# Kernel optimization log

Measured on AMD Instinct MI355X. Metric: run time of the kernel, lower is better.

Reference implementation:

```python
import jax, jax.numpy as jnp
import numpy as np

DIM = 768
HEADS = 12
HEAD_DIM = DIM // HEADS
SCALE = HEAD_DIM ** -0.5


def setup_inputs() -> dict:
    key = jax.random.key(0)
    ks = jax.random.split(key, 6)
    B, N, M, C = 4, 2048, 1024, DIM
    x = jax.random.normal(ks[0], (B, N, C), dtype=jnp.float32)
    r = jax.random.normal(ks[1], (B, M, C), dtype=jnp.float32)
    s = 1.0 / np.sqrt(C)
    W_q = jax.random.normal(ks[2], (C, C), dtype=jnp.float32) * s
    W_kv = jax.random.normal(ks[3], (C, 2 * C), dtype=jnp.float32) * s
    W_proj = jax.random.normal(ks[4], (C, C), dtype=jnp.float32) * s
    b_proj = jax.random.normal(ks[5], (C,), dtype=jnp.float32) * 0.02
    return {"x": x, "r": r, "W_q": W_q, "W_kv": W_kv, "W_proj": W_proj, "b_proj": b_proj}


def reference(x, r, W_q, W_kv, W_proj, b_proj):
    B, N, C = x.shape
    _, M, _ = r.shape
    H, D = HEADS, C // HEADS
    # projections (no bias on q/kv per qkv_bias=False)
    q = (x @ W_q).reshape(B, N, H, D)            # bnhd
    kv = (r @ W_kv).reshape(B, M, 2, H, D)
    k = kv[:, :, 0]                               # bmhd
    v = kv[:, :, 1]                               # bmhd
    attn = jnp.einsum('bnhd,bmhd->bhnm', q, k) * SCALE
    attn = jax.nn.softmax(attn, axis=-1)
    out = jnp.einsum('bhnm,bmhd->bnhd', attn, v).reshape(B, N, C)
    return out @ W_proj + b_proj
```

## Files before the change

### kernel.cpp

```cpp
#include <hip/hip_runtime.h>
#include <hip/hip_bf16.h>
#include <cstdint>

#define HEADS 12

typedef __attribute__((ext_vector_type(8))) __bf16 bf16x8;
typedef __attribute__((ext_vector_type(4))) __bf16 bf16x4;
typedef __attribute__((ext_vector_type(4))) float f32x4;
typedef __attribute__((ext_vector_type(16))) float f32x16;

#define AS1 __attribute__((address_space(1)))
#define AS3 __attribute__((address_space(3)))

__device__ __forceinline__ void gload16(const void* src, void* lds) {
  __builtin_amdgcn_global_load_lds((AS1 void*)src, (AS3 void*)lds, 16, 0, 0);
}

__device__ __forceinline__ uint32_t cvtpk(float lo, float hi) {
  uint32_t r;
  asm("v_cvt_pk_bf16_f32 %0, %1, %2" : "=v"(r) : "v"(lo), "v"(hi));
  return r;
}

__device__ __forceinline__ float exp2_fast(float x) {
  float r;
  asm("v_exp_f32 %0, %1" : "=v"(r) : "v"(x));
  return r;
}

__global__ void k_cast2(const float* __restrict__ x, const float* __restrict__ r,
                        __bf16* __restrict__ xb, __bf16* __restrict__ rb) {
  int i = (blockIdx.x * 256 + threadIdx.x) * 4;
  const float* src;
  __bf16* dst;
  int off;
  if (i < 6291456) { src = x; dst = xb; off = i; }
  else             { src = r; dst = rb; off = i - 6291456; }
  float4 v = *(const float4*)(src + off);
  bf16x4 o;
  o[0] = (__bf16)v.x; o[1] = (__bf16)v.y; o[2] = (__bf16)v.z; o[3] = (__bf16)v.w;
  *(bf16x4*)(dst + off) = o;
}

__global__ void k_twc3(const float* __restrict__ Wq, const float* __restrict__ Wkv,
                       const float* __restrict__ Wp, __bf16* __restrict__ wqt,
                       __bf16* __restrict__ wkvt, __bf16* __restrict__ wpt) {
  __shared__ float tile[32][33];
  const float* W; __bf16* Wt; int N; float scale;
  if (blockIdx.z == 0)      { W = Wq;  Wt = wqt;  N = 768;  scale = 0.18033688011112042f; }
  else if (blockIdx.z == 1) { W = Wkv; Wt = wkvt; N = 1536; scale = 1.0f; }
  else                      { W = Wp;  Wt = wpt;  N = 768;  scale = 1.0f; }
  int nt = blockIdx.x, kt = blockIdx.y;
  if (nt * 32 >= N) return;
  int c = threadIdx.x & 31, r0 = threadIdx.x >> 5;
#pragma unroll
  for (int i = 0; i < 4; ++i) {
    int r = r0 + i * 8;
    tile[r][c] = W[(size_t)(kt * 32 + r) * N + nt * 32 + c];
  }
  __syncthreads();
#pragma unroll
  for (int i = 0; i < 4; ++i) {
    int r = r0 + i * 8;
    Wt[(size_t)(nt * 32 + r) * 768 + kt * 32 + c] = (__bf16)(tile[c][r] * scale);
  }
}

__global__ __launch_bounds__(256, 2) void k_gemm12(
    const __bf16* __restrict__ xb, const __bf16* __restrict__ rb,
    const __bf16* __restrict__ wqt, const __bf16* __restrict__ wkvt,
    __bf16* __restrict__ qb, __bf16* __restrict__ kbp, __bf16* __restrict__ vbp) {
  __shared__ __align__(16) char ldsA[2][16384];
  __shared__ __align__(16) char ldsB[2][16384];
  const int tid = threadIdx.x;
  const int ln = tid & 63;
  const int w = tid >> 6;
  int id = blockIdx.x;
  id = (id & 7) * 96 + (id >> 3);
  const __bf16* A; const __bf16* Bt; int bm0, bn0; bool qpart;
  if (id < 384) { A = xb; Bt = wqt;  bm0 = (id / 6) * 128;  bn0 = (id % 6) * 128;  qpart = true; }
  else { int i2 = id - 384; A = rb; Bt = wkvt; bm0 = (i2 / 12) * 128; bn0 = (i2 % 12) * 128; qpart = false; }
  const int wm0 = (w >> 1) * 64, wn0 = (w & 1) * 64;

  auto stage = [&](char* lds, const __bf16* G, int row0, int k0) {
    const char* gb = (const char*)(G + (size_t)row0 * 768 + k0);
#pragma unroll
    for (int c = 0; c < 4; ++c) {
      int off = c * 4096 + tid * 16;
      int row = off >> 7;
      int s = ((off >> 4) & 7) ^ (row & 7);
      gload16(gb + (size_t)row * 1536 + (s << 4), lds + c * 4096 + (w << 10));
    }
  };

  f32x4 acc[4][4] = {};
  stage(ldsA[0], A, bm0, 0);
  stage(ldsB[0], Bt, bn0, 0);
  __syncthreads();
  for (int kt = 0; kt < 12; ++kt) {
    const char* bufA = ldsA[kt & 1];
    const char* bufB = ldsB[kt & 1];
    if (kt + 1 < 12) {
      stage(ldsA[(kt + 1) & 1], A, bm0, (kt + 1) << 6);
      stage(ldsB[(kt + 1) & 1], Bt, bn0, (kt + 1) << 6);
    }
    bf16x8 af[2][4], bf[2][4];
#pragma unroll
    for (int kk = 0; kk < 2; ++kk)
#pragma unroll
      for (int mt = 0; mt < 4; ++mt) {
        int row = wm0 + mt * 16 + (ln & 15);
        af[kk][mt] = *(const bf16x8*)(bufA + row * 128 + (((kk * 4 + (ln >> 4)) ^ (row & 7)) << 4));
      }
#pragma unroll
    for (int kk = 0; kk < 2; ++kk)
#pragma unroll
      for (int nt = 0; nt < 4; ++nt) {
        int row = wn0 + nt * 16 + (ln & 15);
        bf[kk][nt] = *(const bf16x8*)(bufB + row * 128 + (((kk * 4 + (ln >> 4)) ^ (row & 7)) << 4));
      }
    __builtin_amdgcn_s_setprio(1);
#pragma unroll
    for (int kk = 0; kk < 2; ++kk)
#pragma unroll
      for (int mt = 0; mt < 4; ++mt)
#pragma unroll
        for (int nt = 0; nt < 4; ++nt)
          acc[mt][nt] = __builtin_amdgcn_mfma_f32_16x16x32_bf16(af[kk][mt], bf[kk][nt], acc[mt][nt], 0, 0, 0);
    __builtin_amdgcn_s_setprio(0);
    __syncthreads();
  }

  char* ldsT = &ldsA[0][0];
  const bool vpart = (!qpart) && (bn0 >= 768);
  if (!vpart) {
#pragma unroll
    for (int mt = 0; mt < 4; ++mt)
#pragma unroll
      for (int nt = 0; nt < 4; ++nt)
#pragma unroll
        for (int jj = 0; jj < 4; ++jj) {
          int rowl = wm0 + mt * 16 + ((ln >> 4) << 2) + jj;
          int colb = (wn0 + nt * 16 + (ln & 15)) * 2;
          *(__bf16*)(ldsT + rowl * 256 + (colb ^ ((rowl & 7) << 4))) = (__bf16)acc[mt][nt][jj];
        }
  } else {
#pragma unroll
    for (int mt = 0; mt < 4; ++mt)
#pragma unroll
      for (int nt = 0; nt < 4; ++nt)
#pragma unroll
        for (int jj = 0; jj < 4; ++jj) {
          int dloc = wn0 + nt * 16 + (ln & 15);
          int kvb = (wm0 + mt * 16 + ((ln >> 4) << 2) + jj) * 2;
          *(__bf16*)(ldsT + dloc * 256 + (kvb ^ ((dloc & 7) << 4))) = (__bf16)acc[mt][nt][jj];
        }
  }
  __syncthreads();

  if (qpart) {
#pragma unroll
    for (int it = 0; it < 8; ++it) {
      int rowl = it * 16 + (tid >> 4);
      int colb = (tid & 15) * 16;
      bf16x8 v = *(const bf16x8*)(ldsT + rowl * 256 + (colb ^ ((rowl & 7) << 4)));
      *(bf16x8*)(qb + (size_t)(bm0 + rowl) * 768 + bn0 + (tid & 15) * 8) = v;
    }
  } else if (!vpart) {
    const int bb = bm0 >> 10, kvb0 = (bm0 & 1023) >> 5, hh0 = bn0 >> 6;
#pragma unroll
    for (int it = 0; it < 8; ++it) {
      int hh = it >> 2, t32 = it & 3;
      int dc = tid >> 5, kvl = tid & 31;
      int rowl = t32 * 32 + kvl;
      int colb = hh * 128 + (dc >> 1) * 32 + (dc & 1) * 16;
      bf16x8 v = *(const bf16x8*)(ldsT + rowl * 256 + (colb ^ ((rowl & 7) << 4)));
      *(bf16x8*)(kbp + ((size_t)(bb * 12 + hh0 + hh) * 32 + kvb0 + t32) * 2048 + tid * 8) = v;
    }
  } else {
    const int bb = bm0 >> 10, kvb0 = (bm0 & 1023) >> 5, hh0 = (bn0 - 768) >> 6;
#pragma unroll
    for (int it = 0; it < 8; ++it) {
      int hh = it >> 2, t32 = it & 3;
      int d = ((tid >> 7) << 5) + (tid & 31);
      int kvl8 = (((tid >> 6) & 1) << 4) + (((tid >> 5) & 1) << 3);
      int dloc = hh * 64 + d;
      int kvb = (t32 * 32 + kvl8) * 2;
      bf16x8 v = *(const bf16x8*)(ldsT + dloc * 256 + (kvb ^ ((dloc & 7) << 4)));
      *(bf16x8*)(vbp + ((size_t)(bb * 12 + hh0 + hh) * 32 + kvb0 + t32) * 2048 + tid * 8) = v;
    }
  }
}

__global__ __launch_bounds__(256, 2) void k_gemmP(
    const __bf16* __restrict__ A, const __bf16* __restrict__ Bt,
    float* __restrict__ C, const float* __restrict__ bias) {
  __shared__ __align__(16) char ldsA[2][16384];
  __shared__ __align__(16) char ldsB[2][16384];
  const int tid = threadIdx.x;
  const int ln = tid & 63;
  const int w = tid >> 6;
  int bid = blockIdx.y * 6 + blockIdx.x;
  bid = (bid & 7) * 48 + (bid >> 3);
  const int bm0 = (bid / 6) * 128, bn0 = (bid % 6) * 128;
  const int wm0 = (w >> 1) * 64, wn0 = (w & 1) * 64;

  auto stage = [&](char* lds, const __bf16* G, int row0, int k0) {
    const char* gb = (const char*)(G + (size_t)row0 * 768 + k0);
#pragma unroll
    for (int c = 0; c < 4; ++c) {
      int off = c * 4096 + tid * 16;
      int row = off >> 7;
      int s = ((off >> 4) & 7) ^ (row & 7);
      gload16(gb + (size_t)row * 1536 + (s << 4), lds + c * 4096 + (w << 10));
    }
  };

  f32x4 acc[4][4] = {};
  stage(ldsA[0], A, bm0, 0);
  stage(ldsB[0], Bt, bn0, 0);
  __syncthreads();
  for (int kt = 0; kt < 12; ++kt) {
    const char* bufA = ldsA[kt & 1];
    const char* bufB = ldsB[kt & 1];
    if (kt + 1 < 12) {
      stage(ldsA[(kt + 1) & 1], A, bm0, (kt + 1) << 6);
      stage(ldsB[(kt + 1) & 1], Bt, bn0, (kt + 1) << 6);
    }
    bf16x8 af[2][4], bf[2][4];
#pragma unroll
    for (int kk = 0; kk < 2; ++kk)
#pragma unroll
      for (int mt = 0; mt < 4; ++mt) {
        int row = wm0 + mt * 16 + (ln & 15);
        af[kk][mt] = *(const bf16x8*)(bufA + row * 128 + (((kk * 4 + (ln >> 4)) ^ (row & 7)) << 4));
      }
#pragma unroll
    for (int kk = 0; kk < 2; ++kk)
#pragma unroll
      for (int nt = 0; nt < 4; ++nt) {
        int row = wn0 + nt * 16 + (ln & 15);
        bf[kk][nt] = *(const bf16x8*)(bufB + row * 128 + (((kk * 4 + (ln >> 4)) ^ (row & 7)) << 4));
      }
    __builtin_amdgcn_s_setprio(1);
#pragma unroll
    for (int kk = 0; kk < 2; ++kk)
#pragma unroll
      for (int mt = 0; mt < 4; ++mt)
#pragma unroll
        for (int nt = 0; nt < 4; ++nt)
          acc[mt][nt] = __builtin_amdgcn_mfma_f32_16x16x32_bf16(af[kk][mt], bf[kk][nt], acc[mt][nt], 0, 0, 0);
    __builtin_amdgcn_s_setprio(0);
    __syncthreads();
  }
#pragma unroll
  for (int mt = 0; mt < 4; ++mt) {
    int row = bm0 + wm0 + mt * 16 + ((ln >> 4) << 2);
#pragma unroll
    for (int nt = 0; nt < 4; ++nt) {
      int col = bn0 + wn0 + nt * 16 + (ln & 15);
      float bv = bias[col];
#pragma unroll
      for (int jj = 0; jj < 4; ++jj)
        C[(size_t)(row + jj) * 768 + col] = acc[mt][nt][jj] + bv;
    }
  }
}

__global__ __launch_bounds__(128, 3) void k_attn(
    const __bf16* __restrict__ q, const __bf16* __restrict__ kb,
    const __bf16* __restrict__ vb, __bf16* __restrict__ ao) {
  __shared__ __align__(16) char ldsK[3][8192];
  const int tid = threadIdx.x, ln = tid & 63;
  const int l5 = ln >> 5, l32 = ln & 31, w = tid >> 6;
  int id = blockIdx.x;
  id = (id & 7) * 192 + (id >> 3);
  const int qt = id & 31, bh = id >> 5;
  const int b = bh / HEADS, h = bh % HEADS;
  const int qrow = b * 2048 + qt * 64 + w * 32 + l32;

  const char* kbase = (const char*)kb + (size_t)bh * 131072;
  const __bf16* vbase = vb + (size_t)bh * 65536;
  const int vchunk = l5 * 256 + l32 * 8;

  auto stageK = [&](int t, int buf) {
#pragma unroll
    for (int c = 0; c < 4; ++c)
      gload16(kbase + (size_t)t * 8192 + c * 2048 + tid * 16, ldsK[buf] + c * 2048 + tid * 16);
  };

  bf16x8 qf[4];
#pragma unroll
  for (int s = 0; s < 4; ++s)
    qf[s] = *(const bf16x8*)(q + (size_t)qrow * 768 + h * 64 + 16 * s + 8 * l5);

  stageK(0, 0);
  stageK(1, 1);

  f32x16 accO[2] = {};
  float mrow = -1e30f, lrow = 0.f;

  asm volatile("s_waitcnt vmcnt(0)" ::: "memory");
  __builtin_amdgcn_s_barrier();

  for (int t = 0; t < 16; ++t) {
    const char* bufK = ldsK[t % 3];

    bf16x8 vf[2][2][2];
    {
      const __bf16* vt = vbase + (size_t)(2 * t) * 2048 + vchunk;
#pragma unroll
      for (int nt = 0; nt < 2; ++nt)
#pragma unroll
        for (int dt = 0; dt < 2; ++dt)
#pragma unroll
          for (int ks = 0; ks < 2; ++ks)
            vf[nt][dt][ks] = *(const bf16x8*)(vt + nt * 2048 + (dt * 2 + ks) * 512);
    }
    if (t < 14) stageK(t + 2, (t + 2) % 3);

    f32x16 s16[2] = {};
    __builtin_amdgcn_s_setprio(1);
#pragma unroll
    for (int s = 0; s < 4; ++s) {
      bf16x8 kf0 = *(const bf16x8*)(bufK + (s * 2 + l5) * 512 + l32 * 16);
      s16[0] = __builtin_amdgcn_mfma_f32_32x32x16_bf16(kf0, qf[s], s16[0], 0, 0, 0);
      bf16x8 kf1 = *(const bf16x8*)(bufK + 4096 + (s * 2 + l5) * 512 + l32 * 16);
      s16[1] = __builtin_amdgcn_mfma_f32_32x32x16_bf16(kf1, qf[s], s16[1], 0, 0, 0);
    }
    __builtin_amdgcn_s_setprio(0);

    float lm = s16[0][0];
#pragma unroll
    for (int nt = 0; nt < 2; ++nt)
#pragma unroll
      for (int i = 0; i < 16; ++i) lm = fmaxf(lm, s16[nt][i]);
    if (!__all(lm <= mrow + 8.0f)) {
      float mx = fmaxf(lm, __shfl_xor(lm, 32, 64));
      float mn = fmaxf(mrow, mx);
      float corr = exp2_fast(mrow - mn);
      mrow = mn;
      lrow *= corr;
#pragma unroll
      for (int dt = 0; dt < 2; ++dt)
#pragma unroll
        for (int i = 0; i < 16; ++i) accO[dt][i] *= corr;
    }
    float ps = 0.f;
#pragma unroll
    for (int nt = 0; nt < 2; ++nt)
#pragma unroll
      for (int i = 0; i < 16; ++i) {
        float e = exp2_fast(s16[nt][i] - mrow);
        s16[nt][i] = e;
        ps += e;
      }
    lrow += ps;

    bf16x8 pk[2][2];
#pragma unroll
    for (int nt = 0; nt < 2; ++nt) {
      uint32_t c0[4], c1[4];
#pragma unroll
      for (int j = 0; j < 4; ++j) {
        c0[j] = cvtpk(s16[nt][4 * j], s16[nt][4 * j + 1]);
        c1[j] = cvtpk(s16[nt][4 * j + 2], s16[nt][4 * j + 3]);
      }
      uint32_t w00 = c0[0], w02 = c0[1];
      asm("v_permlane32_swap_b32 %0, %1" : "+v"(w00), "+v"(w02));
      uint32_t w01 = c1[0], w03 = c1[1];
      asm("v_permlane32_swap_b32 %0, %1" : "+v"(w01), "+v"(w03));
      uint32_t w10 = c0[2], w12 = c0[3];
      asm("v_permlane32_swap_b32 %0, %1" : "+v"(w10), "+v"(w12));
      uint32_t w11 = c1[2], w13 = c1[3];
      asm("v_permlane32_swap_b32 %0, %1" : "+v"(w11), "+v"(w13));
      union { uint32_t u[4]; bf16x8 v; } pk0, pk1;
      pk0.u[0] = w00; pk0.u[1] = w01; pk0.u[2] = w02; pk0.u[3] = w03;
      pk1.u[0] = w10; pk1.u[1] = w11; pk1.u[2] = w12; pk1.u[3] = w13;
      pk[nt][0] = pk0.v;
      pk[nt][1] = pk1.v;
    }

    __builtin_amdgcn_s_setprio(1);
#pragma unroll
    for (int nt = 0; nt < 2; ++nt)
#pragma unroll
      for (int ks = 0; ks < 2; ++ks) {
        accO[0] = __builtin_amdgcn_mfma_f32_32x32x16_bf16(vf[nt][0][ks], pk[nt][ks], accO[0], 0, 0, 0);
        accO[1] = __builtin_amdgcn_mfma_f32_32x32x16_bf16(vf[nt][1][ks], pk[nt][ks], accO[1], 0, 0, 0);
      }
    __builtin_amdgcn_s_setprio(0);

    __builtin_amdgcn_sched_barrier(0);
    __builtin_amdgcn_s_barrier();
  }

  float l = lrow + __shfl_xor(lrow, 32, 64);
  float inv = 1.0f / l;
  size_t rowb = (size_t)qrow * 768 + h * 64;
#pragma unroll
  for (int dt = 0; dt < 2; ++dt)
#pragma unroll
    for (int j = 0; j < 4; ++j) {
      bf16x4 o;
#pragma unroll
      for (int i = 0; i < 4; ++i) o[i] = (__bf16)(accO[dt][4 * j + i] * inv);
      *(bf16x4*)(ao + rowb + dt * 32 + 8 * j + 4 * l5) = o;
    }
}

extern "C" void kernel_launch(void* const* d_in, const int* in_sizes, int n_in,
                              void* d_out, int out_size, void* d_ws, size_t ws_size,
                              hipStream_t stream) {
  const float* x = (const float*)d_in[0];
  const float* r = (const float*)d_in[1];
  const float* Wq = (const float*)d_in[2];
  const float* Wkv = (const float*)d_in[3];
  const float* Wp = (const float*)d_in[4];
  const float* bp = (const float*)d_in[5];

  char* ws = (char*)d_ws;
  __bf16* xb  = (__bf16*)ws; ws += (size_t)6291456 * 2;
  __bf16* rb  = (__bf16*)ws; ws += (size_t)3145728 * 2;
  __bf16* wqt = (__bf16*)ws; ws += (size_t)589824 * 2;
  __bf16* wkvt= (__bf16*)ws; ws += (size_t)1179648 * 2;
  __bf16* wpt = (__bf16*)ws; ws += (size_t)589824 * 2;
  __bf16* qb  = (__bf16*)ws; ws += (size_t)6291456 * 2;
  __bf16* kbk = (__bf16*)ws; ws += (size_t)3145728 * 2;
  __bf16* vbk = (__bf16*)ws; ws += (size_t)3145728 * 2;
  __bf16* ao  = (__bf16*)ws;

  k_cast2<<<9216, 256, 0, stream>>>(x, r, xb, rb);
  k_twc3<<<dim3(48, 24, 3), 256, 0, stream>>>(Wq, Wkv, Wp, wqt, wkvt, wpt);
  k_gemm12<<<768, 256, 0, stream>>>(xb, rb, wqt, wkvt, qb, kbk, vbk);
  k_attn<<<1536, 128, 0, stream>>>(qb, kbk, vbk, ao);
  k_gemmP<<<dim3(6, 64), 256, 0, stream>>>(ao, wpt, (float*)d_out, bp);
}
```

Baseline: 100.9 us.

## Software-pipeline attention loop: compute next QK tile before softmax/PV of current

Restructures the flash-attention inner loop into a two-stage software pipeline. The QK^T MFMAs for tile t+1 are issued right after the softmax/PV of tile t, using ping-pong score registers and an unroll by two. This is meant to overlap the softmax VALU work and the V loads with MFMA work and cut per-tile stalls. It raises register pressure through the second score buffer, and the changed barrier placement with the 3-buffer K staging has to stay race-free.

```diff
diff --git a/kernel.cpp b/kernel.cpp
--- a/kernel.cpp
+++ b/kernel.cpp
@@ -299,42 +299,41 @@
 
   f32x16 accO[2] = {};
   float mrow = -1e30f, lrow = 0.f;
-
-  asm volatile("s_waitcnt vmcnt(0)" ::: "memory");
-  __builtin_amdgcn_s_barrier();
-
-  for (int t = 0; t < 16; ++t) {
+  bf16x8 vf[8];
+
+  auto loadV = [&](int t) {
+    const __bf16* vt = vbase + (size_t)(2 * t) * 2048 + vchunk;
+#pragma unroll
+    for (int nt = 0; nt < 2; ++nt)
+#pragma unroll
+      for (int dt = 0; dt < 2; ++dt)
+#pragma unroll
+        for (int ks = 0; ks < 2; ++ks)
+          vf[nt * 4 + dt * 2 + ks] = *(const bf16x8*)(vt + nt * 2048 + (dt * 2 + ks) * 512);
+  };
+
+  auto QK = [&](int t, f32x16& s0, f32x16& s1) {
     const char* bufK = ldsK[t % 3];
-
-    bf16x8 vf[2][2][2];
-    {
-      const __bf16* vt = vbase + (size_t)(2 * t) * 2048 + vchunk;
-#pragma unroll
-      for (int nt = 0; nt < 2; ++nt)
-#pragma unroll
-        for (int dt = 0; dt < 2; ++dt)
-#pragma unroll
-          for (int ks = 0; ks < 2; ++ks)
-            vf[nt][dt][ks] = *(const bf16x8*)(vt + nt * 2048 + (dt * 2 + ks) * 512);
-    }
-    if (t < 14) stageK(t + 2, (t + 2) % 3);
-
-    f32x16 s16[2] = {};
+    f32x16 r0 = {}, r1 = {};
     __builtin_amdgcn_s_setprio(1);
 #pragma unroll
     for (int s = 0; s < 4; ++s) {
       bf16x8 kf0 = *(const bf16x8*)(bufK + (s * 2 + l5) * 512 + l32 * 16);
-      s16[0] = __builtin_amdgcn_mfma_f32_32x32x16_bf16(kf0, qf[s], s16[0], 0, 0, 0);
+      r0 = __builtin_amdgcn_mfma_f32_32x32x16_bf16(kf0, qf[s], r0, 0, 0, 0);
       bf16x8 kf1 = *(const bf16x8*)(bufK + 4096 + (s * 2 + l5) * 512 + l32 * 16);
-      s16[1] = __builtin_amdgcn_mfma_f32_32x32x16_bf16(kf1, qf[s], s16[1], 0, 0, 0);
+      r1 = __builtin_amdgcn_mfma_f32_32x32x16_bf16(kf1, qf[s], r1, 0, 0, 0);
     }
     __builtin_amdgcn_s_setprio(0);
-
-    float lm = s16[0][0];
-#pragma unroll
-    for (int nt = 0; nt < 2; ++nt)
-#pragma unroll
-      for (int i = 0; i < 16; ++i) lm = fmaxf(lm, s16[nt][i]);
+    s0 = r0;
+    s1 = r1;
+  };
+
+  auto SMPV = [&](f32x16& t0, f32x16& t1) {
+    float lm = t0[0];
+#pragma unroll
+    for (int i = 0; i < 16; ++i) lm = fmaxf(lm, t0[i]);
+#pragma unroll
+    for (int i = 0; i < 16; ++i) lm = fmaxf(lm, t1[i]);
     if (!__all(lm <= mrow + 8.0f)) {
       float mx = fmaxf(lm, __shfl_xor(lm, 32, 64));
       float mn = fmaxf(mrow, mx);
@@ -348,23 +347,20 @@
     }
     float ps = 0.f;
 #pragma unroll
-    for (int nt = 0; nt < 2; ++nt)
-#pragma unroll
-      for (int i = 0; i < 16; ++i) {
-        float e = exp2_fast(s16[nt][i] - mrow);
-        s16[nt][i] = e;
-        ps += e;
-      }
+    for (int i = 0; i < 16; ++i) { float e = exp2_fast(t0[i] - mrow); t0[i] = e; ps += e; }
+#pragma unroll
+    for (int i = 0; i < 16; ++i) { float e = exp2_fast(t1[i] - mrow); t1[i] = e; ps += e; }
     lrow += ps;
 
     bf16x8 pk[2][2];
 #pragma unroll
     for (int nt = 0; nt < 2; ++nt) {
+      const f32x16& sv = nt ? t1 : t0;
       uint32_t c0[4], c1[4];
 #pragma unroll
       for (int j = 0; j < 4; ++j) {
-        c0[j] = cvtpk(s16[nt][4 * j], s16[nt][4 * j + 1]);
-        c1[j] = cvtpk(s16[nt][4 * j + 2], s16[nt][4 * j + 3]);
+        c0[j] = cvtpk(sv[4 * j], sv[4 * j + 1]);
+        c1[j] = cvtpk(sv[4 * j + 2], sv[4 * j + 3]);
       }
       uint32_t w00 = c0[0], w02 = c0[1];
       asm("v_permlane32_swap_b32 %0, %1" : "+v"(w00), "+v"(w02));
@@ -386,12 +382,37 @@
     for (int nt = 0; nt < 2; ++nt)
 #pragma unroll
       for (int ks = 0; ks < 2; ++ks) {
-        accO[0] = __builtin_amdgcn_mfma_f32_32x32x16_bf16(vf[nt][0][ks], pk[nt][ks], accO[0], 0, 0, 0);
-        accO[1] = __builtin_amdgcn_mfma_f32_32x32x16_bf16(vf[nt][1][ks], pk[nt][ks], accO[1], 0, 0, 0);
+        accO[0] = __builtin_amdgcn_mfma_f32_32x32x16_bf16(vf[nt * 4 + ks], pk[nt][ks], accO[0], 0, 0, 0);
+        accO[1] = __builtin_amdgcn_mfma_f32_32x32x16_bf16(vf[nt * 4 + 2 + ks], pk[nt][ks], accO[1], 0, 0, 0);
       }
     __builtin_amdgcn_s_setprio(0);
-
+  };
+
+  asm volatile("s_waitcnt vmcnt(0)" ::: "memory");
+  __builtin_amdgcn_s_barrier();
+
+  f32x16 sA0, sA1, sB0, sB1;
+  loadV(0);
+  stageK(2, 2);
+  QK(0, sA0, sA1);
+  __builtin_amdgcn_s_barrier();
+
+#pragma unroll
+  for (int i = 0; i < 8; ++i) {
+    const int tA = 2 * i, tB = 2 * i + 1;
+    SMPV(sA0, sA1);
+    loadV(tA + 1);
+    if (tA + 3 < 16) stageK(tA + 3, (tA + 3) % 3);
     __builtin_amdgcn_sched_barrier(0);
+    QK(tB, sB0, sB1);
+    __builtin_amdgcn_s_barrier();
+    SMPV(sB0, sB1);
+    if (tB < 15) {
+      loadV(tB + 1);
+      if (tB + 3 < 16) stageK(tB + 3, (tB + 3) % 3);
+      __builtin_amdgcn_sched_barrier(0);
+      QK(tB + 1, sA0, sA1);
+    }
     __builtin_amdgcn_s_barrier();
   }
 
```

New measurement: 101.0 us. Within noise of the previous version (+0.1%).
